# Performance work log

Measured on AMD Instinct MI355X. Metric: run time of the kernel, lower is better.

The kernel has to match this reference:

```python
import jax, jax.numpy as jnp
import numpy as np

B, S, D = 2, 2048, 1024
H, DH = 16, 64  # n_heads, d_head = d_model // n_heads


def setup_inputs() -> dict:
    key = jax.random.key(0)
    ks = jax.random.split(key, 12)
    scale = 1.0 / np.sqrt(D)
    return {
        "queries": jax.random.normal(ks[0], (B, S, D), jnp.float32),
        "keys": jax.random.normal(ks[1], (B, S, D), jnp.float32),
        "values": jax.random.normal(ks[2], (B, S, D), jnp.float32),
        "mask": jax.random.randint(ks[3], (1, 1, S, S), 0, 2, jnp.int32),
        "Wq": jax.random.normal(ks[4], (D, D), jnp.float32) * scale,
        "bq": jnp.zeros((D,), jnp.float32),
        "Wk": jax.random.normal(ks[5], (D, D), jnp.float32) * scale,
        "bk": jnp.zeros((D,), jnp.float32),
        "Wv": jax.random.normal(ks[6], (D, D), jnp.float32) * scale,
        "bv": jnp.zeros((D,), jnp.float32),
        "Wo": jax.random.normal(ks[7], (D, D), jnp.float32) * scale,
        "bo": jnp.zeros((D,), jnp.float32),
    }


def _split_proj(x):
    # (B, ?, H, DH) reshape then permute -> (B, H, ?, DH)
    b = x.shape[0]
    return x.reshape(b, -1, H, DH).transpose(0, 2, 1, 3)


def reference(queries, keys, values, mask, Wq, bq, Wk, bk, Wv, bv, Wo, bo):
    q = queries @ Wq.T + bq
    k = keys @ Wk.T + bk
    v = values @ Wv.T + bv
    # NOTE: original source applies split_proj to queries twice (faithful repro)
    q = _split_proj(_split_proj(q))
    k = _split_proj(k)
    v = _split_proj(v)
    scores = jnp.einsum('bhqd,bhkd->bhqk', q, k) / jnp.sqrt(jnp.float32(DH))
    scores = scores + mask.astype(scores.dtype) * (-1e9)
    attn = jax.nn.softmax(scores, axis=-1)
    out = jnp.einsum('bhqk,bhkd->bhqd', attn, v)  # (B,H,S,DH)
    out = out.transpose(0, 2, 1, 3).reshape(out.shape[0], -1, D)
    return out @ Wo.T + bo
```

## Files before the change

### kernel.cpp

```cpp
#include <hip/hip_runtime.h>
#include <hip/hip_bf16.h>
#include <cstddef>
#include <cstdint>


typedef __attribute__((ext_vector_type(8))) short bf16x8;
typedef __attribute__((ext_vector_type(4))) float f32x4;

__device__ __forceinline__ void gl_lds16(const void* g, void* l) {
    __builtin_amdgcn_global_load_lds(
        (const __attribute__((address_space(1))) void*)g,
        (__attribute__((address_space(3))) void*)l, 16, 0, 0);
}

__device__ __forceinline__ int4 cvt8(const float* __restrict__ src) {
    const float4 v0 = *(const float4*)src, v1 = *(const float4*)(src + 4);
    union { __hip_bfloat16 h[8]; int4 q; } u;
    u.h[0] = __float2bfloat16(v0.x); u.h[1] = __float2bfloat16(v0.y);
    u.h[2] = __float2bfloat16(v0.z); u.h[3] = __float2bfloat16(v0.w);
    u.h[4] = __float2bfloat16(v1.x); u.h[5] = __float2bfloat16(v1.y);
    u.h[6] = __float2bfloat16(v1.z); u.h[7] = __float2bfloat16(v1.w);
    return u.q;
}

__global__ __launch_bounds__(256) void convert_all(
    const float* __restrict__ q, const float* __restrict__ k, const float* __restrict__ v,
    const float* __restrict__ wq, const float* __restrict__ wk,
    const float* __restrict__ wv, const float* __restrict__ wo,
    __hip_bfloat16* __restrict__ dq, __hip_bfloat16* __restrict__ dk,
    __hip_bfloat16* __restrict__ dv, __hip_bfloat16* __restrict__ dwq,
    __hip_bfloat16* __restrict__ dwk, __hip_bfloat16* __restrict__ dwv,
    __hip_bfloat16* __restrict__ dwo)
{
    const int bid = blockIdx.x;
    const float* s; __hip_bfloat16* d; int base;
    if      (bid < 2048) { s = q;  d = dq;  base = bid; }
    else if (bid < 4096) { s = k;  d = dk;  base = bid - 2048; }
    else if (bid < 6144) { s = v;  d = dv;  base = bid - 4096; }
    else if (bid < 6656) { s = wq; d = dwq; base = bid - 6144; }
    else if (bid < 7168) { s = wk; d = dwk; base = bid - 6656; }
    else if (bid < 7680) { s = wv; d = dwv; base = bid - 7168; }
    else                 { s = wo; d = dwo; base = bid - 7680; }
    const size_t i = (size_t)base * 256 + threadIdx.x;
    *((int4*)d + i) = cvt8(s + i * 8);
}

__global__ __launch_bounds__(256) void packmask(const int* __restrict__ mask,
                                                unsigned long long* __restrict__ mbits)
{
    const int wid  = (blockIdx.x * 256 + threadIdx.x) >> 6;
    const int lane = threadIdx.x & 63;
    const int qr = wid >> 5, w64 = wid & 31;
    const int m = mask[(size_t)qr * 2048 + w64 * 64 + lane];
    const unsigned long long bal = __ballot(m != 0);
    if (lane == 0) mbits[(size_t)qr * 32 + w64] = bal;
}

template <int MR, typename OutT>
__device__ __forceinline__ void gemm_body(
    const __hip_bfloat16* __restrict__ A, const __hip_bfloat16* __restrict__ Bm,
    const float* __restrict__ bias, OutT* __restrict__ C,
    int N, int m0, int n0, int brow,
    __hip_bfloat16* As, __hip_bfloat16* Bs)
{
    const int t = threadIdx.x, lane = t & 63, w = t >> 6;
    const int l15 = lane & 15, g = lane >> 4;
    const int wr = w >> 1, wc = w & 1;
    constexpr int NI = MR / 32;

    f32x4 acc[NI][4] = {};

    for (int k0 = 0; k0 < 1024; k0 += 64) {
        __syncthreads();
        #pragma unroll
        for (int it = 0; it < NI; ++it) {
            const int c = it * 256 + t, row = c >> 3, c8 = c & 7;
            gl_lds16(A + (size_t)(m0 + row) * 1024 + k0 + c8 * 8, (char*)As + c * 16);
        }
        #pragma unroll
        for (int it = 0; it < 4; ++it) {
            const int c = it * 256 + t, row = c >> 3, c8 = c & 7;
            gl_lds16(Bm + (size_t)(n0 + row) * 1024 + k0 + c8 * 8, (char*)Bs + c * 16);
        }
        __syncthreads();
        #pragma unroll
        for (int kk = 0; kk < 64; kk += 32) {
            bf16x8 af[NI], bfr[4];
            #pragma unroll
            for (int i = 0; i < NI; ++i)
                af[i] = *(const bf16x8*)((const char*)As + (wr * (MR / 2) + i * 16 + l15) * 128 + kk * 2 + g * 16);
            #pragma unroll
            for (int j = 0; j < 4; ++j)
                bfr[j] = *(const bf16x8*)((const char*)Bs + (wc * 64 + j * 16 + l15) * 128 + kk * 2 + g * 16);
            #pragma unroll
            for (int i = 0; i < NI; ++i)
                #pragma unroll
                for (int j = 0; j < 4; ++j)
                    acc[i][j] = __builtin_amdgcn_mfma_f32_16x16x32_bf16(af[i], bfr[j], acc[i][j], 0, 0, 0);
        }
    }

    #pragma unroll
    for (int i = 0; i < NI; ++i) {
        const int m = m0 + wr * (MR / 2) + i * 16 + g * 4;
        #pragma unroll
        for (int j = 0; j < 4; ++j) {
            const int n = n0 + wc * 64 + j * 16 + l15;
            const float bc = brow ? 0.f : bias[n];
            #pragma unroll
            for (int r = 0; r < 4; ++r) {
                const float v = acc[i][j][r] + (brow ? bias[m + r] : bc);
                C[(size_t)(m + r) * N + n] = (OutT)v;
            }
        }
    }
}

__global__ __launch_bounds__(256) void qkv_gemm(
    const __hip_bfloat16* __restrict__ qin, const __hip_bfloat16* __restrict__ kin,
    const __hip_bfloat16* __restrict__ vin,
    const __hip_bfloat16* __restrict__ Wqb, const __hip_bfloat16* __restrict__ Wkb,
    const __hip_bfloat16* __restrict__ Wvb,
    const float* __restrict__ bq, const float* __restrict__ bk, const float* __restrict__ bv,
    __hip_bfloat16* __restrict__ qbuf, __hip_bfloat16* __restrict__ kbuf,
    __hip_bfloat16* __restrict__ vtb)
{
    __shared__ __align__(16) __hip_bfloat16 As[128 * 64];
    __shared__ __align__(16) __hip_bfloat16 Bs[128 * 64];
    const int z = blockIdx.z;
    if (z == 0)
        gemm_body<128>(qin, Wqb, bq, qbuf, 1024, blockIdx.y * 128, blockIdx.x * 128, 0, As, Bs);
    else if (z == 1)
        gemm_body<128>(kin, Wkb, bk, kbuf, 1024, blockIdx.y * 128, blockIdx.x * 128, 0, As, Bs);
    else
        gemm_body<128>(Wvb, vin, bv, vtb, 4096, blockIdx.x * 128, blockIdx.y * 128, 1, As, Bs);
}

__global__ __launch_bounds__(256) void out_gemm(
    const __hip_bfloat16* __restrict__ A, const __hip_bfloat16* __restrict__ Bm,
    const float* __restrict__ bias, float* __restrict__ C)
{
    __shared__ __align__(16) __hip_bfloat16 As[64 * 64];
    __shared__ __align__(16) __hip_bfloat16 Bs[128 * 64];
    gemm_body<64>(A, Bm, bias, C, 1024, blockIdx.y * 64, blockIdx.x * 128, 0, As, Bs);
}

__global__ __launch_bounds__(512, 4) void attn_mfma(
    const __hip_bfloat16* __restrict__ qb,
    const __hip_bfloat16* __restrict__ kb,
    const __hip_bfloat16* __restrict__ vt,
    const unsigned long long* __restrict__ mbits,
    __hip_bfloat16* __restrict__ ctx)
{
    __shared__ __align__(16) char smem[65536];

    const int t = threadIdx.x, lane = t & 63, w = t >> 6;
    const int grp = w >> 2, wl = w & 3;
    const int l15 = lane & 15, g = lane >> 4;
    const int tloc = t & 255;

    const int bid = blockIdx.x;
    const int xcd = bid & 7, ii = bid >> 3;
    const int bh = (xcd << 2) + (ii >> 4), qt = ii & 15;
    const int b = bh >> 4, a = bh & 15;
    const int q0 = qt * 128;
    const int kt0 = grp * 16;

    constexpr float SC_LOG2E = 0.18033688011112042f;
    constexpr float OFFC     = -17.312340490667561f;
    constexpr float MASKB    = -1.0e9f;

    bf16x8 qreg[2][2];
    int qgl[2];
    #pragma unroll
    for (int u = 0; u < 2; ++u) {
        const int qg = q0 + wl * 32 + u * 16 + l15;
        qgl[u] = qg;
        const int srow = (qg & 127) * 16 + a;
        #pragma unroll
        for (int half = 0; half < 2; ++half)
            qreg[u][half] = *(const bf16x8*)&qb[(size_t)(b * 2048 + srow) * 1024 + qt * 64 + (half * 4 + g) * 8];
    }

    const int srow0 = tloc >> 3, scc = tloc & 7;
    const int scs = scc ^ (srow0 & 7);
    const char* kSrc = (const char*)(kb + (size_t)(b * 2048 + kt0 * 64 + srow0) * 1024 + a * 64 + scs * 8);
    const char* vSrc = (const char*)(vt + (size_t)(a * 64 + srow0) * 4096 + b * 2048 + kt0 * 64 + scs * 8);
    char* kDst = smem + grp * 16384 + tloc * 16;
    char* vDst = smem + 32768 + grp * 16384 + tloc * 16;

    auto stage = [&](int bufn) {
        gl_lds16(kSrc,          kDst + bufn * 8192);
        gl_lds16(kSrc + 65536,  kDst + bufn * 8192 + 4096);
        gl_lds16(vSrc,          vDst + bufn * 8192);
        gl_lds16(vSrc + 262144, vDst + bufn * 8192 + 4096);
        kSrc += 131072;
        vSrc += 128;
    };

    int kofs[2][4], vofs[2][4];
    #pragma unroll
    for (int x = 0; x < 2; ++x)
        #pragma unroll
        for (int nf = 0; nf < 4; ++nf) {
            const int rr = nf * 16 + l15;
            const int sw = ((x * 4 + g) ^ (rr & 7)) << 4;
            kofs[x][nf] = grp * 16384 + rr * 128 + sw;
            vofs[x][nf] = 32768 + grp * 16384 + rr * 128 + sw;
        }

    const unsigned long long* mbP0 = mbits + (size_t)qgl[0] * 32 + kt0;
    const unsigned long long* mbP1 = mbits + (size_t)qgl[1] * 32 + kt0;

    bf16x8 ones;
    #pragma unroll
    for (int e = 0; e < 8; ++e) ones[e] = (short)0x3F80;

    f32x4 accd[2][4] = {};
    f32x4 accl[2] = {};

    stage(0);
    __syncthreads();

    auto do_tile = [&](int buf, bool doStage) {
        if (doStage) stage(buf ^ 1);
        const uint2 mw0 = *(const uint2*)mbP0; ++mbP0;
        const uint2 mw1 = *(const uint2*)mbP1; ++mbP1;

        f32x4 sf[2][4] = {};
        #pragma unroll
        for (int half = 0; half < 2; ++half)
            #pragma unroll
            for (int nf = 0; nf < 4; ++nf) {
                const bf16x8 kf = *(const bf16x8*)(smem + kofs[half][nf] + buf * 8192);
                sf[0][nf] = __builtin_amdgcn_mfma_f32_16x16x32_bf16(kf, qreg[0][half], sf[0][nf], 0, 0, 0);
                sf[1][nf] = __builtin_amdgcn_mfma_f32_16x16x32_bf16(kf, qreg[1][half], sf[1][nf], 0, 0, 0);
            }

        unsigned Wrd[2][4][2];
        #pragma unroll
        for (int u = 0; u < 2; ++u) {
            const uint2 mwv = u ? mw1 : mw0;
            #pragma unroll
            for (int nf = 0; nf < 4; ++nf) {
                const unsigned word = (nf & 2) ? mwv.y : mwv.x;
                const int bsh = ((nf & 1) << 4) + (g << 2);
                float pr[4];
                #pragma unroll
                for (int r = 0; r < 4; ++r) {
                    const bool msk = (word >> (bsh + r)) & 1u;
                    pr[r] = __builtin_amdgcn_exp2f(
                        fmaf(sf[u][nf][r], SC_LOG2E, msk ? MASKB : OFFC));
                }
                Wrd[u][nf][0] = ((__float_as_uint(pr[1]) + 0x8000u) & 0xffff0000u)
                              | ((__float_as_uint(pr[0]) + 0x8000u) >> 16);
                Wrd[u][nf][1] = ((__float_as_uint(pr[3]) + 0x8000u) & 0xffff0000u)
                              | ((__float_as_uint(pr[2]) + 0x8000u) >> 16);
            }
        }

        #pragma unroll
        for (int jj = 0; jj < 2; ++jj) {
            bf16x8 paf[2];
            #pragma unroll
            for (int u = 0; u < 2; ++u) {
                unsigned f0 = Wrd[u][2 * jj][0], f2 = Wrd[u][2 * jj + 1][0];
                unsigned f1 = Wrd[u][2 * jj][1], f3 = Wrd[u][2 * jj + 1][1];
                asm volatile("v_permlane32_swap_b32 %0, %1" : "+v"(f0), "+v"(f2));
                asm volatile("v_permlane16_swap_b32 %0, %1" : "+v"(f0), "+v"(f2));
                asm volatile("v_permlane32_swap_b32 %0, %1" : "+v"(f1), "+v"(f3));
                asm volatile("v_permlane16_swap_b32 %0, %1" : "+v"(f1), "+v"(f3));
                union { unsigned uw[4]; bf16x8 v; } uu;
                uu.uw[0] = f0; uu.uw[1] = f1; uu.uw[2] = f2; uu.uw[3] = f3;
                paf[u] = uu.v;
                accl[u] = __builtin_amdgcn_mfma_f32_16x16x32_bf16(paf[u], ones, accl[u], 0, 0, 0);
            }
            #pragma unroll
            for (int df = 0; df < 4; ++df) {
                const bf16x8 vf = *(const bf16x8*)(smem + vofs[jj][df] + buf * 8192);
                accd[0][df] = __builtin_amdgcn_mfma_f32_16x16x32_bf16(paf[0], vf, accd[0][df], 0, 0, 0);
                accd[1][df] = __builtin_amdgcn_mfma_f32_16x16x32_bf16(paf[1], vf, accd[1][df], 0, 0, 0);
            }
        }
        __syncthreads();
    };

    #pragma unroll 1
    for (int it2 = 0; it2 < 8; ++it2) {
        do_tile(0, true);
        do_tile(1, it2 != 7);
    }

    float* cmbO = (float*)smem;
    float* cmbL = (float*)(smem + 32768);
    if (grp == 0) {
        #pragma unroll
        for (int u = 0; u < 2; ++u)
            #pragma unroll
            for (int r = 0; r < 4; ++r) {
                const int row = wl * 32 + u * 16 + (g << 2) + r;
                #pragma unroll
                for (int df = 0; df < 4; ++df)
                    cmbO[row * 64 + df * 16 + l15] = accd[u][df][r];
                if (l15 == 0) cmbL[row] = accl[u][r];
            }
    }
    __syncthreads();
    if (grp == 1) {
        #pragma unroll
        for (int u = 0; u < 2; ++u)
            #pragma unroll
            for (int r = 0; r < 4; ++r) {
                const int row = wl * 32 + u * 16 + (g << 2) + r;
                const float lsum = accl[u][r] + cmbL[row];
                const float inv = 1.0f / lsum;
                const int qglob = q0 + row;
                #pragma unroll
                for (int df = 0; df < 4; ++df) {
                    const float o = accd[u][df][r] + cmbO[row * 64 + df * 16 + l15];
                    ctx[(size_t)(b * 2048 + qglob) * 1024 + (a << 6) + df * 16 + l15] =
                        __float2bfloat16(o * inv);
                }
            }
    }
}

extern "C" void kernel_launch(void* const* d_in, const int* in_sizes, int n_in,
                              void* d_out, int out_size, void* d_ws, size_t ws_size,
                              hipStream_t stream)
{
    const float* queries = (const float*)d_in[0];
    const float* keys    = (const float*)d_in[1];
    const float* values  = (const float*)d_in[2];
    const int*   mask    = (const int*)  d_in[3];
    const float* Wq = (const float*)d_in[4];
    const float* bq = (const float*)d_in[5];
    const float* Wk = (const float*)d_in[6];
    const float* bk = (const float*)d_in[7];
    const float* Wv = (const float*)d_in[8];
    const float* bv = (const float*)d_in[9];
    const float* Wo = (const float*)d_in[10];
    const float* bo = (const float*)d_in[11];

    const size_t NM = (size_t)4096 * 1024;
    const size_t NW = (size_t)1024 * 1024;
    __hip_bfloat16* p = (__hip_bfloat16*)d_ws;
    __hip_bfloat16* qin = p;  p += NM;
    __hip_bfloat16* kin = p;  p += NM;
    __hip_bfloat16* vin = p;  p += NM;
    __hip_bfloat16* Wqb = p;  p += NW;
    __hip_bfloat16* Wkb = p;  p += NW;
    __hip_bfloat16* Wvb = p;  p += NW;
    __hip_bfloat16* Wob = p;  p += NW;
    __hip_bfloat16* qbuf = p; p += NM;
    __hip_bfloat16* kbuf = p; p += NM;
    __hip_bfloat16* vtb  = p; p += NM;
    unsigned long long* mbits = (unsigned long long*)p;
    __hip_bfloat16* ctxb = qin;

    convert_all<<<dim3(8192), dim3(256), 0, stream>>>(
        queries, keys, values, Wq, Wk, Wv, Wo,
        qin, kin, vin, Wqb, Wkb, Wvb, Wob);
    packmask<<<dim3(16384), dim3(256), 0, stream>>>(mask, mbits);

    qkv_gemm<<<dim3(8, 32, 3), dim3(256), 0, stream>>>(
        qin, kin, vin, Wqb, Wkb, Wvb, bq, bk, bv, qbuf, kbuf, vtb);

    attn_mfma<<<dim3(512), dim3(512), 0, stream>>>(qbuf, kbuf, vtb, mbits, ctxb);

    out_gemm<<<dim3(8, 64), dim3(256), 0, stream>>>(ctxb, Wob, bo, (float*)d_out);
}
```

Before: 162.9 us.

## Merge convert and mask-pack kernels, add MFMA priority hints, use perm packing

Folds the mask bit-packing kernel into the fp32-to-bf16 conversion kernel so one launch does both, removing a kernel launch and its tail. In the attention inner loop, the MFMA sections are wrapped in s_setprio(1)/s_setprio(0) so waves issuing matrix ops get scheduling priority. The bf16 pack of the softmax probabilities now uses a single v_perm byte select instead of separate mask/shift/or operations. The changes are independent small tweaks and carry little correctness risk.

```diff
diff --git a/kernel.cpp b/kernel.cpp
--- a/kernel.cpp
+++ b/kernel.cpp
@@ -23,16 +23,27 @@
     return u.q;
 }
 
-__global__ __launch_bounds__(256) void convert_all(
+__global__ __launch_bounds__(256) void prep(
     const float* __restrict__ q, const float* __restrict__ k, const float* __restrict__ v,
     const float* __restrict__ wq, const float* __restrict__ wk,
     const float* __restrict__ wv, const float* __restrict__ wo,
+    const int* __restrict__ mask,
     __hip_bfloat16* __restrict__ dq, __hip_bfloat16* __restrict__ dk,
     __hip_bfloat16* __restrict__ dv, __hip_bfloat16* __restrict__ dwq,
     __hip_bfloat16* __restrict__ dwk, __hip_bfloat16* __restrict__ dwv,
-    __hip_bfloat16* __restrict__ dwo)
+    __hip_bfloat16* __restrict__ dwo,
+    unsigned long long* __restrict__ mbits)
 {
     const int bid = blockIdx.x;
+    if (bid >= 8192) {
+        const int wid  = ((bid - 8192) * 256 + threadIdx.x) >> 6;
+        const int lane = threadIdx.x & 63;
+        const int qr = wid >> 5, w64 = wid & 31;
+        const int m = mask[(size_t)qr * 2048 + w64 * 64 + lane];
+        const unsigned long long bal = __ballot(m != 0);
+        if (lane == 0) mbits[(size_t)qr * 32 + w64] = bal;
+        return;
+    }
     const float* s; __hip_bfloat16* d; int base;
     if      (bid < 2048) { s = q;  d = dq;  base = bid; }
     else if (bid < 4096) { s = k;  d = dk;  base = bid - 2048; }
@@ -45,17 +56,6 @@
     *((int4*)d + i) = cvt8(s + i * 8);
 }
 
-__global__ __launch_bounds__(256) void packmask(const int* __restrict__ mask,
-                                                unsigned long long* __restrict__ mbits)
-{
-    const int wid  = (blockIdx.x * 256 + threadIdx.x) >> 6;
-    const int lane = threadIdx.x & 63;
-    const int qr = wid >> 5, w64 = wid & 31;
-    const int m = mask[(size_t)qr * 2048 + w64 * 64 + lane];
-    const unsigned long long bal = __ballot(m != 0);
-    if (lane == 0) mbits[(size_t)qr * 32 + w64] = bal;
-}
-
 template <int MR, typename OutT>
 __device__ __forceinline__ void gemm_body(
     const __hip_bfloat16* __restrict__ A, const __hip_bfloat16* __restrict__ Bm,
@@ -228,6 +228,7 @@
         const uint2 mw1 = *(const uint2*)mbP1; ++mbP1;
 
         f32x4 sf[2][4] = {};
+        __builtin_amdgcn_s_setprio(1);
         #pragma unroll
         for (int half = 0; half < 2; ++half)
             #pragma unroll
@@ -236,6 +237,7 @@
                 sf[0][nf] = __builtin_amdgcn_mfma_f32_16x16x32_bf16(kf, qreg[0][half], sf[0][nf], 0, 0, 0);
                 sf[1][nf] = __builtin_amdgcn_mfma_f32_16x16x32_bf16(kf, qreg[1][half], sf[1][nf], 0, 0, 0);
             }
+        __builtin_amdgcn_s_setprio(0);
 
         unsigned Wrd[2][4][2];
         #pragma unroll
@@ -252,10 +254,12 @@
                     pr[r] = __builtin_amdgcn_exp2f(
                         fmaf(sf[u][nf][r], SC_LOG2E, msk ? MASKB : OFFC));
                 }
-                Wrd[u][nf][0] = ((__float_as_uint(pr[1]) + 0x8000u) & 0xffff0000u)
-                              | ((__float_as_uint(pr[0]) + 0x8000u) >> 16);
-                Wrd[u][nf][1] = ((__float_as_uint(pr[3]) + 0x8000u) & 0xffff0000u)
-                              | ((__float_as_uint(pr[2]) + 0x8000u) >> 16);
+                Wrd[u][nf][0] = __builtin_amdgcn_perm(
+                    __float_as_uint(pr[1]) + 0x8000u,
+                    __float_as_uint(pr[0]) + 0x8000u, 0x07060302u);
+                Wrd[u][nf][1] = __builtin_amdgcn_perm(
+                    __float_as_uint(pr[3]) + 0x8000u,
+                    __float_as_uint(pr[2]) + 0x8000u, 0x07060302u);
             }
         }
 
@@ -273,14 +277,18 @@
                 union { unsigned uw[4]; bf16x8 v; } uu;
                 uu.uw[0] = f0; uu.uw[1] = f1; uu.uw[2] = f2; uu.uw[3] = f3;
                 paf[u] = uu.v;
+            }
+            __builtin_amdgcn_s_setprio(1);
+            #pragma unroll
+            for (int u = 0; u < 2; ++u)
                 accl[u] = __builtin_amdgcn_mfma_f32_16x16x32_bf16(paf[u], ones, accl[u], 0, 0, 0);
-            }
             #pragma unroll
             for (int df = 0; df < 4; ++df) {
                 const bf16x8 vf = *(const bf16x8*)(smem + vofs[jj][df] + buf * 8192);
                 accd[0][df] = __builtin_amdgcn_mfma_f32_16x16x32_bf16(paf[0], vf, accd[0][df], 0, 0, 0);
                 accd[1][df] = __builtin_amdgcn_mfma_f32_16x16x32_bf16(paf[1], vf, accd[1][df], 0, 0, 0);
             }
+            __builtin_amdgcn_s_setprio(0);
         }
         __syncthreads();
     };
@@ -358,10 +366,9 @@
     unsigned long long* mbits = (unsigned long long*)p;
     __hip_bfloat16* ctxb = qin;
 
-    convert_all<<<dim3(8192), dim3(256), 0, stream>>>(
-        queries, keys, values, Wq, Wk, Wv, Wo,
-        qin, kin, vin, Wqb, Wkb, Wvb, Wob);
-    packmask<<<dim3(16384), dim3(256), 0, stream>>>(mask, mbits);
+    prep<<<dim3(24576), dim3(256), 0, stream>>>(
+        queries, keys, values, Wq, Wk, Wv, Wo, mask,
+        qin, kin, vin, Wqb, Wkb, Wvb, Wob, mbits);
 
     qkv_gemm<<<dim3(8, 32, 3), dim3(256), 0, stream>>>(
         qin, kin, vin, Wqb, Wkb, Wvb, bq, bk, bv, qbuf, kbuf, vtb);
```

New measurement: 166.6 us. +2.2%, slower.
